# Performance work log

Hardware: AMD Instinct MI355X
Metric: run time of the kernel (lower is better)

The kernel has to match this reference:

```python
import jax, jax.numpy as jnp
import numpy as np

B, S, D = 2, 2048, 2048
H, HKV, DH = 16, 4, 128   # query heads, kv heads, head dim
N_REP = H // HKV
ROPE_BASE = 10000.0


def rotate_half(x):
    x1, x2 = x[..., : DH // 2], x[..., DH // 2 :]
    return jnp.concatenate((-x2, x1), axis=-1)


def rope_tables(seq_len, dtype=jnp.float32):
    inv_freq = 1.0 / (ROPE_BASE ** (jnp.arange(0, DH, 2, dtype=jnp.float32) / DH))
    t = jnp.arange(seq_len, dtype=jnp.float32)
    freqs = jnp.outer(t, inv_freq)                 # [S, DH/2]
    emb = jnp.concatenate((freqs, freqs), axis=-1)  # [S, DH]
    return jnp.cos(emb).astype(dtype), jnp.sin(emb).astype(dtype)


def setup_inputs() -> dict:
    key = jax.random.key(0)
    k1, k2, k3, k4, k5 = jax.random.split(key, 5)
    scale = 1.0 / np.sqrt(D)
    return {
        "hidden_states": jax.random.normal(k1, (B, S, D), dtype=jnp.float32),
        "position_ids": jnp.tile(jnp.arange(S, dtype=jnp.int32)[None, :], (B, 1)),
        "wq": jax.random.normal(k2, (D, H * DH), dtype=jnp.float32) * scale,
        "wk": jax.random.normal(k3, (D, HKV * DH), dtype=jnp.float32) * scale,
        "wv": jax.random.normal(k4, (D, HKV * DH), dtype=jnp.float32) * scale,
        "wo": jax.random.normal(k5, (H * DH, D), dtype=jnp.float32) * scale,
    }


def reference(hidden_states, position_ids, wq, wk, wv, wo):
    x = hidden_states
    b, s, _ = x.shape

    # QKV projections -> [B, H(kv), S, DH]
    q = (x @ wq).reshape(b, s, H, DH).transpose(0, 2, 1, 3)
    k = (x @ wk).reshape(b, s, HKV, DH).transpose(0, 2, 1, 3)
    v = (x @ wv).reshape(b, s, HKV, DH).transpose(0, 2, 1, 3)

    # Rotary position embedding
    cos_t, sin_t = rope_tables(s, x.dtype)
    cos = cos_t[position_ids][:, None, :, :]  # [B,1,S,DH]
    sin = sin_t[position_ids][:, None, :, :]
    q = q * cos + rotate_half(q) * sin
    k = k * cos + rotate_half(k) * sin

    # GQA: repeat KV heads to match query heads
    k = jnp.repeat(k, N_REP, axis=1)  # [B,H,S,DH]
    v = jnp.repeat(v, N_REP, axis=1)

    # Causal SDPA
    scores = jnp.einsum("bhqd,bhkd->bhqk", q, k) / jnp.sqrt(
        jnp.asarray(DH, x.dtype)
    )
    causal = jnp.tril(jnp.ones((s, s), dtype=bool))
    scores = jnp.where(causal[None, None], scores, jnp.asarray(-1e9, x.dtype))
    attn = jax.nn.softmax(scores, axis=-1)
    out = jnp.einsum("bhqk,bhkd->bhqd", attn, v)  # [B,H,S,DH]

    out = out.transpose(0, 2, 1, 3).reshape(b, s, H * DH)
    return out @ wo
```

## Files before the change

kernel.cpp:

```cpp
#include <hip/hip_runtime.h>
#include <cmath>

typedef unsigned short u16;
typedef float floatx4 __attribute__((ext_vector_type(4)));
typedef short short8 __attribute__((ext_vector_type(8)));
typedef short short4v __attribute__((ext_vector_type(4)));
typedef __bf16 bf16x8 __attribute__((ext_vector_type(8)));

#define GLOBAL_AS __attribute__((address_space(1)))
#define LDS_AS __attribute__((address_space(3)))

#define S_LEN 2048
#define D_MODEL 2048
#define NH 16
#define NKV 4
#define DHEAD 128
#define SM_SCALE 0.08838834764831843f
#define K2 (SM_SCALE * 1.4426950408889634f)

__device__ __forceinline__ u16 f2bf(float f) {
    unsigned int u = __builtin_bit_cast(unsigned int, f);
    u += 0x7fffu + ((u >> 16) & 1u);
    return (u16)(u >> 16);
}
__device__ __forceinline__ u16 f2bfr(float f) {
    unsigned int u = __builtin_bit_cast(unsigned int, f);
    return (u16)((u + 0x8000u) >> 16);
}
__device__ __forceinline__ float bf2f(u16 x) {
    unsigned int u = ((unsigned int)x) << 16;
    return __builtin_bit_cast(float, u);
}
__device__ __forceinline__ floatx4 zf4() {
    floatx4 z; z[0] = 0.f; z[1] = 0.f; z[2] = 0.f; z[3] = 0.f; return z;
}
__device__ __forceinline__ floatx4 mfma16(short8 a, short8 b, floatx4 c) {
    return __builtin_amdgcn_mfma_f32_16x16x32_bf16(
        __builtin_bit_cast(bf16x8, a), __builtin_bit_cast(bf16x8, b), c, 0, 0, 0);
}
__device__ __forceinline__ floatx4 mfma16k16(short4v a, short4v b, floatx4 c) {
    return __builtin_amdgcn_mfma_f32_16x16x16bf16_1k(a, b, c, 0, 0, 0);
}
__device__ __forceinline__ void async16(const u16* g, u16* l) {
    __builtin_amdgcn_global_load_lds((GLOBAL_AS void*)g, (LDS_AS void*)l, 16, 0, 0);
}

__global__ void cast_x_kernel(const float4* __restrict__ in, ushort4* __restrict__ out) {
    int i = blockIdx.x * 256 + threadIdx.x;
    float4 v = in[i];
    ushort4 o;
    o.x = f2bf(v.x); o.y = f2bf(v.y); o.z = f2bf(v.z); o.w = f2bf(v.w);
    out[i] = o;
}

__global__ void transpose_cast_kernel(const float* __restrict__ in, u16* __restrict__ out,
                                      int R, int C) {
    __shared__ float tile[32][33];
    int tx = threadIdx.x & 31, ty = threadIdx.x >> 5;
    int bx = blockIdx.x * 32;
    int by = blockIdx.y * 32;
#pragma unroll
    for (int i = 0; i < 32; i += 8)
        tile[ty + i][tx] = in[(size_t)(by + ty + i) * C + bx + tx];
    __syncthreads();
#pragma unroll
    for (int i = 0; i < 32; i += 8)
        out[(size_t)(bx + ty + i) * R + by + tx] = f2bf(tile[tx][ty + i]);
}

__global__ void rope_tables_kernel(float* __restrict__ cs_tab, float* __restrict__ sn_tab) {
    int idx = blockIdx.x * 256 + threadIdx.x;
    int p = idx >> 6, j = idx & 63;
    double e = (double)(2 * j) / 128.0;
    double invf = pow(10000.0, -e);
    float arg = (float)p * (float)invf;
    cs_tab[idx] = (float)cos((double)arg);
    sn_tab[idx] = (float)sin((double)arg);
}

__global__ void rope_apply_kernel(u16* __restrict__ Qb, u16* __restrict__ Kb,
                                  const int* __restrict__ pos,
                                  const float4* __restrict__ cs_tab,
                                  const float4* __restrict__ sn_tab) {
    int idx = blockIdx.x * 256 + threadIdx.x;
    int j4 = idx & 15;
    int s = (idx >> 4) & 2047;
    int r = idx >> 15;
    int hh = r % 20, b = r / 20;
    int p = pos[b * S_LEN + s];
    float4 cs = cs_tab[p * 16 + j4];
    float4 sn = sn_tab[p * 16 + j4];
    u16* base;
    if (hh < 16) base = Qb + (((size_t)(b * NH + hh)) * S_LEN + s) * DHEAD;
    else         base = Kb + (((size_t)(b * NKV + (hh - 16))) * S_LEN + s) * DHEAD;
    base += j4 * 4;
    ushort4 a = *(const ushort4*)(base);
    ushort4 c = *(const ushort4*)(base + 64);
    ushort4 oa, oc;
    float x1, x2;
    x1 = bf2f(a.x); x2 = bf2f(c.x); oa.x = f2bf(x1 * cs.x - x2 * sn.x); oc.x = f2bf(x2 * cs.x + x1 * sn.x);
    x1 = bf2f(a.y); x2 = bf2f(c.y); oa.y = f2bf(x1 * cs.y - x2 * sn.y); oc.y = f2bf(x2 * cs.y + x1 * sn.y);
    x1 = bf2f(a.z); x2 = bf2f(c.z); oa.z = f2bf(x1 * cs.z - x2 * sn.z); oc.z = f2bf(x2 * cs.z + x1 * sn.z);
    x1 = bf2f(a.w); x2 = bf2f(c.w); oa.w = f2bf(x1 * cs.w - x2 * sn.w); oc.w = f2bf(x2 * cs.w + x1 * sn.w);
    *(ushort4*)(base) = oa;
    *(ushort4*)(base + 64) = oc;
}

__device__ __forceinline__ void gemm_mainloop(const u16* __restrict__ A,
                                              const u16* __restrict__ Bt,
                                              int K, u16* ldsA, u16* ldsB,
                                              floatx4 acc[4][4]) {
    const int t = threadIdx.x;
    const int lane = t & 63, wave = t >> 6;
    const int wr = wave >> 1, wc = wave & 1;
    const int lr = lane & 15, q = lane >> 4;
    const int m0 = blockIdx.y * 128, n0 = blockIdx.x * 128;
    const int swz = q ^ ((lr >> 1) & 3);

#pragma unroll
    for (int r = 0; r < 4; ++r)
#pragma unroll
        for (int c = 0; c < 4; ++c) acc[r][c] = zf4();

    for (int k0 = 0; k0 < K; k0 += 32) {
#pragma unroll
        for (int i = 0; i < 2; ++i) {
            int ci = i * 256 + t;
            int row = ci >> 2;
            int kc = ((ci & 3) ^ ((ci >> 3) & 3)) << 3;
            async16(A + (size_t)(m0 + row) * K + k0 + kc, ldsA + (i * 256 + wave * 64) * 8);
            async16(Bt + (size_t)(n0 + row) * K + k0 + kc, ldsB + (i * 256 + wave * 64) * 8);
        }
        __syncthreads();
        short8 af[4], bfr[4];
#pragma unroll
        for (int r = 0; r < 4; ++r)
            af[r] = *(const short8*)(ldsA + (wr * 64 + r * 16 + lr) * 32 + swz * 8);
#pragma unroll
        for (int c = 0; c < 4; ++c)
            bfr[c] = *(const short8*)(ldsB + (wc * 64 + c * 16 + lr) * 32 + swz * 8);
#pragma unroll
        for (int r = 0; r < 4; ++r)
#pragma unroll
            for (int c = 0; c < 4; ++c)
                acc[r][c] = mfma16(af[r], bfr[c], acc[r][c]);
        __syncthreads();
    }
}

__global__ void qkv_gemm_kernel(const u16* __restrict__ A, const u16* __restrict__ Bt,
                                u16* __restrict__ Qb, u16* __restrict__ Kb,
                                u16* __restrict__ Vt) {
    __shared__ u16 ldsA[128 * 32];
    __shared__ u16 ldsB[128 * 32];
    floatx4 acc[4][4];
    gemm_mainloop(A, Bt, D_MODEL, ldsA, ldsB, acc);

    const int t = threadIdx.x, lane = t & 63, wave = t >> 6;
    const int wr = wave >> 1, wc = wave & 1, lr = lane & 15, q = lane >> 4;
    const int m0 = blockIdx.y * 128 + wr * 64, n0 = blockIdx.x * 128 + wc * 64;
#pragma unroll
    for (int r = 0; r < 4; ++r)
#pragma unroll
        for (int c = 0; c < 4; ++c) {
            int gc = n0 + c * 16 + lr;
#pragma unroll
            for (int rr = 0; rr < 4; ++rr) {
                int grow = m0 + r * 16 + q * 4 + rr;
                int bb = grow >> 11, s = grow & 2047;
                u16 bv = f2bf(acc[r][c][rr]);
                int d = gc & 127;
                if (gc < 2048) {
                    int hh = gc >> 7;
                    Qb[(((size_t)(bb * NH + hh)) * S_LEN + s) * DHEAD + d] = bv;
                } else if (gc < 2560) {
                    int hh = (gc - 2048) >> 7;
                    Kb[(((size_t)(bb * NKV + hh)) * S_LEN + s) * DHEAD + d] = bv;
                } else {
                    int hh = (gc - 2560) >> 7;
                    Vt[(((size_t)(bb * NKV + hh)) * DHEAD + d) * S_LEN + s] = bv;
                }
            }
        }
}

__global__ void out_gemm_kernel(const u16* __restrict__ A, const u16* __restrict__ Bt,
                                float* __restrict__ out) {
    __shared__ u16 ldsA[128 * 32];
    __shared__ u16 ldsB[128 * 32];
    floatx4 acc[4][4];
    gemm_mainloop(A, Bt, D_MODEL, ldsA, ldsB, acc);

    const int t = threadIdx.x, lane = t & 63, wave = t >> 6;
    const int wr = wave >> 1, wc = wave & 1, lr = lane & 15, q = lane >> 4;
    const int m0 = blockIdx.y * 128 + wr * 64, n0 = blockIdx.x * 128 + wc * 64;
#pragma unroll
    for (int r = 0; r < 4; ++r)
#pragma unroll
        for (int c = 0; c < 4; ++c) {
            int gc = n0 + c * 16 + lr;
#pragma unroll
            for (int rr = 0; rr < 4; ++rr) {
                int grow = m0 + r * 16 + q * 4 + rr;
                out[(size_t)grow * D_MODEL + gc] = acc[r][c][rr];
            }
        }
}

__global__ __launch_bounds__(256, 4) void fa_kernel(const u16* __restrict__ Qb,
                                                    const u16* __restrict__ Kb,
                                                    const u16* __restrict__ Vt,
                                                    u16* __restrict__ Ob) {
    __shared__ u16 ldsK[64 * 128];
    __shared__ u16 ldsV[128 * 64];

    const int t = threadIdx.x, lane = t & 63, wave = t >> 6;
    const int lr = lane & 15, q = lane >> 4;
    const int swz = lr & 7;

    const int bid = blockIdx.x;
    const int qt = 31 - (bid >> 5);
    const int bh = bid & 31;
    const int b = bh >> 4, h = bh & 15;
    const int kvh = h >> 2;

    const u16* Kp = Kb + (size_t)(b * NKV + kvh) * S_LEN * DHEAD;
    const u16* Vp = Vt + (size_t)(b * NKV + kvh) * DHEAD * S_LEN;
    const u16* Qp = Qb + ((size_t)((b * NH + h) * S_LEN) + qt * 64 + wave * 16) * DHEAD;

    short8 qf[4];
#pragma unroll
    for (int kk = 0; kk < 4; ++kk)
        qf[kk] = *(const short8*)(Qp + (size_t)lr * DHEAD + kk * 32 + q * 8);

    floatx4 accO[8];
#pragma unroll
    for (int d = 0; d < 8; ++d) accO[d] = zf4();
    float m_i = -3e38f, l_i = 0.f;

    const int nkt = qt + 1;
    for (int kt = 0; kt < nkt; ++kt) {
#pragma unroll
        for (int i = 0; i < 4; ++i) {
            int ci = i * 256 + t;
            int krow = ci >> 4, kc = ((ci & 15) ^ ((ci >> 4) & 7)) << 3;
            async16(Kp + (size_t)(kt * 64 + krow) * DHEAD + kc,
                    ldsK + (i * 256 + wave * 64) * 8);
            int dh = ci >> 3, vc = ((ci & 7) ^ ((ci >> 3) & 7)) << 3;
            async16(Vp + (size_t)dh * S_LEN + kt * 64 + vc,
                    ldsV + (i * 256 + wave * 64) * 8);
        }
        __syncthreads();

        floatx4 sc[4];
#pragma unroll
        for (int c = 0; c < 4; ++c) {
            sc[c] = zf4();
#pragma unroll
            for (int kk = 0; kk < 4; ++kk) {
                short8 kfr = *(const short8*)(ldsK + (c * 16 + lr) * DHEAD +
                                              (((kk * 4 + q) ^ swz) << 3));
                sc[c] = mfma16(kfr, qf[kk], sc[c]);
            }
        }

        if (kt == qt) {
            const int qrow = wave * 16 + lr;
#pragma unroll
            for (int c = 0; c < 4; ++c)
#pragma unroll
                for (int rr = 0; rr < 4; ++rr)
                    if (c * 16 + q * 4 + rr > qrow) sc[c][rr] = -3e38f;
        }

        float mx = -3e38f;
#pragma unroll
        for (int c = 0; c < 4; ++c)
#pragma unroll
            for (int rr = 0; rr < 4; ++rr) mx = fmaxf(mx, sc[c][rr]);
        mx = fmaxf(mx, __shfl_xor(mx, 16));
        mx = fmaxf(mx, __shfl_xor(mx, 32));
        float mnew = fmaxf(m_i, mx);
        float mk = mnew * K2;
        float alpha = __builtin_amdgcn_exp2f(fmaf(m_i, K2, -mk));
        m_i = mnew;
        float rs = 0.f;
#pragma unroll
        for (int c = 0; c < 4; ++c)
#pragma unroll
            for (int rr = 0; rr < 4; ++rr) {
                float p = __builtin_amdgcn_exp2f(fmaf(sc[c][rr], K2, -mk));
                sc[c][rr] = p;
                rs += p;
            }
        rs += __shfl_xor(rs, 16);
        rs += __shfl_xor(rs, 32);
        l_i = l_i * alpha + rs;
#pragma unroll
        for (int d = 0; d < 8; ++d) accO[d] *= alpha;

        short4v pb[4];
#pragma unroll
        for (int c = 0; c < 4; ++c) {
            pb[c][0] = (short)f2bfr(sc[c][0]);
            pb[c][1] = (short)f2bfr(sc[c][1]);
            pb[c][2] = (short)f2bfr(sc[c][2]);
            pb[c][3] = (short)f2bfr(sc[c][3]);
        }

#pragma unroll
        for (int ks = 0; ks < 4; ++ks)
#pragma unroll
            for (int d = 0; d < 8; ++d) {
                short4v vf = *(const short4v*)(ldsV + (d * 16 + lr) * 64 +
                                               (((ks * 2 + (q >> 1)) ^ swz) << 3) +
                                               (q & 1) * 4);
                accO[d] = mfma16k16(vf, pb[ks], accO[d]);
            }
        __syncthreads();
    }

    const int tok = qt * 64 + wave * 16 + lr;
    const float inv = 1.0f / l_i;
    u16* orow = Ob + ((size_t)(b * S_LEN + tok)) * (NH * DHEAD) + h * DHEAD + q * 4;
#pragma unroll
    for (int d = 0; d < 8; ++d) {
        ushort4 o;
        o.x = f2bf(accO[d][0] * inv);
        o.y = f2bf(accO[d][1] * inv);
        o.z = f2bf(accO[d][2] * inv);
        o.w = f2bf(accO[d][3] * inv);
        *(ushort4*)(orow + d * 16) = o;
    }
}

extern "C" void kernel_launch(void* const* d_in, const int* in_sizes, int n_in,
                              void* d_out, int out_size, void* d_ws, size_t ws_size,
                              hipStream_t stream) {
    const float* X  = (const float*)d_in[0];
    const int* pos  = (const int*)d_in[1];
    const float* wq = (const float*)d_in[2];
    const float* wk = (const float*)d_in[3];
    const float* wv = (const float*)d_in[4];
    const float* wo = (const float*)d_in[5];
    float* out = (float*)d_out;

    char* w = (char*)d_ws;
    u16* Xbf    = (u16*)(w);
    u16* Wqkv   = (u16*)(w + 16777216);
    u16* Wo     = (u16*)(w + 29360128);
    u16* Qb     = (u16*)(w + 37748736);
    u16* Kb     = (u16*)(w + 54525952);
    u16* Vt     = (u16*)(w + 58720256);
    u16* Ob     = (u16*)(w + 62914560);
    float* cst  = (float*)(w + 79691776);
    float* snt  = (float*)(w + 80216064);

    cast_x_kernel<<<8192, 256, 0, stream>>>((const float4*)X, (ushort4*)Xbf);
    transpose_cast_kernel<<<dim3(64, 64), 256, 0, stream>>>(wq, Wqkv, 2048, 2048);
    transpose_cast_kernel<<<dim3(16, 64), 256, 0, stream>>>(wk, Wqkv + (size_t)2048 * 2048, 2048, 512);
    transpose_cast_kernel<<<dim3(16, 64), 256, 0, stream>>>(wv, Wqkv + (size_t)2560 * 2048, 2048, 512);
    transpose_cast_kernel<<<dim3(64, 64), 256, 0, stream>>>(wo, Wo, 2048, 2048);
    rope_tables_kernel<<<512, 256, 0, stream>>>(cst, snt);
    qkv_gemm_kernel<<<dim3(24, 32), 256, 0, stream>>>(Xbf, Wqkv, Qb, Kb, Vt);
    rope_apply_kernel<<<5120, 256, 0, stream>>>(Qb, Kb, pos, (const float4*)cst, (const float4*)snt);
    fa_kernel<<<1024, 256, 0, stream>>>(Qb, Kb, Vt, Ob);
    out_gemm_kernel<<<dim3(16, 32), 256, 0, stream>>>(Ob, Wo, out);
}
```

Baseline: 326.3 us.

## Deepen GEMM K-tile, reorder attention blocks, skip redundant rescale, swizzle V layout

The shared GEMM mainloop now stages 64-wide K tiles, using a new 8-way XOR swizzle and two MFMA sub-steps per barrier pair, which halves the number of barriers and LDS refill rounds. The flash-attention grid is remapped so that each group of blocks pairs short and long causal query tiles, which should balance work across CUs. The online-softmax rescale of the accumulator is skipped when no row max increased in the wave. V is written with an XOR of the sequence index so that the half-16-byte reads in attention hit fewer LDS bank conflicts. Together these raise LDS usage and add some index arithmetic.

```diff
diff --git a/kernel.cpp b/kernel.cpp
--- a/kernel.cpp
+++ b/kernel.cpp
@@ -115,35 +115,40 @@
     const int wr = wave >> 1, wc = wave & 1;
     const int lr = lane & 15, q = lane >> 4;
     const int m0 = blockIdx.y * 128, n0 = blockIdx.x * 128;
-    const int swz = q ^ ((lr >> 1) & 3);
+    const int swz = lr & 7;
 
 #pragma unroll
     for (int r = 0; r < 4; ++r)
 #pragma unroll
         for (int c = 0; c < 4; ++c) acc[r][c] = zf4();
 
-    for (int k0 = 0; k0 < K; k0 += 32) {
-#pragma unroll
-        for (int i = 0; i < 2; ++i) {
+    for (int k0 = 0; k0 < K; k0 += 64) {
+#pragma unroll
+        for (int i = 0; i < 4; ++i) {
             int ci = i * 256 + t;
-            int row = ci >> 2;
-            int kc = ((ci & 3) ^ ((ci >> 3) & 3)) << 3;
+            int row = ci >> 3;
+            int kc = ((ci & 7) ^ (row & 7)) << 3;
             async16(A + (size_t)(m0 + row) * K + k0 + kc, ldsA + (i * 256 + wave * 64) * 8);
             async16(Bt + (size_t)(n0 + row) * K + k0 + kc, ldsB + (i * 256 + wave * 64) * 8);
         }
         __syncthreads();
-        short8 af[4], bfr[4];
-#pragma unroll
-        for (int r = 0; r < 4; ++r)
-            af[r] = *(const short8*)(ldsA + (wr * 64 + r * 16 + lr) * 32 + swz * 8);
-#pragma unroll
-        for (int c = 0; c < 4; ++c)
-            bfr[c] = *(const short8*)(ldsB + (wc * 64 + c * 16 + lr) * 32 + swz * 8);
-#pragma unroll
-        for (int r = 0; r < 4; ++r)
+#pragma unroll
+        for (int ks = 0; ks < 2; ++ks) {
+            short8 af[4], bfr[4];
+#pragma unroll
+            for (int r = 0; r < 4; ++r)
+                af[r] = *(const short8*)(ldsA + (wr * 64 + r * 16 + lr) * 64 +
+                                         (((ks * 4 + q) ^ swz) << 3));
 #pragma unroll
             for (int c = 0; c < 4; ++c)
-                acc[r][c] = mfma16(af[r], bfr[c], acc[r][c]);
+                bfr[c] = *(const short8*)(ldsB + (wc * 64 + c * 16 + lr) * 64 +
+                                          (((ks * 4 + q) ^ swz) << 3));
+#pragma unroll
+            for (int r = 0; r < 4; ++r)
+#pragma unroll
+                for (int c = 0; c < 4; ++c)
+                    acc[r][c] = mfma16(af[r], bfr[c], acc[r][c]);
+        }
         __syncthreads();
     }
 }
@@ -151,8 +156,8 @@
 __global__ void qkv_gemm_kernel(const u16* __restrict__ A, const u16* __restrict__ Bt,
                                 u16* __restrict__ Qb, u16* __restrict__ Kb,
                                 u16* __restrict__ Vt) {
-    __shared__ u16 ldsA[128 * 32];
-    __shared__ u16 ldsB[128 * 32];
+    __shared__ u16 ldsA[128 * 64];
+    __shared__ u16 ldsB[128 * 64];
     floatx4 acc[4][4];
     gemm_mainloop(A, Bt, D_MODEL, ldsA, ldsB, acc);
 
@@ -178,7 +183,8 @@
                     Kb[(((size_t)(bb * NKV + hh)) * S_LEN + s) * DHEAD + d] = bv;
                 } else {
                     int hh = (gc - 2560) >> 7;
-                    Vt[(((size_t)(bb * NKV + hh)) * DHEAD + d) * S_LEN + s] = bv;
+                    int s2 = s ^ ((d & 8) >> 1);
+                    Vt[(((size_t)(bb * NKV + hh)) * DHEAD + d) * S_LEN + s2] = bv;
                 }
             }
         }
@@ -186,8 +192,8 @@
 
 __global__ void out_gemm_kernel(const u16* __restrict__ A, const u16* __restrict__ Bt,
                                 float* __restrict__ out) {
-    __shared__ u16 ldsA[128 * 32];
-    __shared__ u16 ldsB[128 * 32];
+    __shared__ u16 ldsA[128 * 64];
+    __shared__ u16 ldsB[128 * 64];
     floatx4 acc[4][4];
     gemm_mainloop(A, Bt, D_MODEL, ldsA, ldsB, acc);
 
@@ -219,8 +225,14 @@
     const int swz = lr & 7;
 
     const int bid = blockIdx.x;
-    const int qt = 31 - (bid >> 5);
-    const int bh = bid & 31;
+    const int r4 = bid >> 8, j = bid & 255;
+    const int p = j >> 3, lo = j & 7;
+    const int bh = r4 * 8 + lo;
+    int qt;
+    if (r4 == 0) qt = p;
+    else if (r4 == 1) qt = 31 - p;
+    else if (r4 == 2) qt = p ^ 16;
+    else qt = 31 - (p ^ 16);
     const int b = bh >> 4, h = bh & 15;
     const int kvh = h >> 2;
 
@@ -282,22 +294,27 @@
         mx = fmaxf(mx, __shfl_xor(mx, 32));
         float mnew = fmaxf(m_i, mx);
         float mk = mnew * K2;
-        float alpha = __builtin_amdgcn_exp2f(fmaf(m_i, K2, -mk));
-        m_i = mnew;
+        bool anyup = __any(mnew > m_i);
         float rs = 0.f;
 #pragma unroll
         for (int c = 0; c < 4; ++c)
 #pragma unroll
             for (int rr = 0; rr < 4; ++rr) {
-                float p = __builtin_amdgcn_exp2f(fmaf(sc[c][rr], K2, -mk));
-                sc[c][rr] = p;
-                rs += p;
+                float pe = __builtin_amdgcn_exp2f(fmaf(sc[c][rr], K2, -mk));
+                sc[c][rr] = pe;
+                rs += pe;
             }
         rs += __shfl_xor(rs, 16);
         rs += __shfl_xor(rs, 32);
-        l_i = l_i * alpha + rs;
-#pragma unroll
-        for (int d = 0; d < 8; ++d) accO[d] *= alpha;
+        if (anyup) {
+            float alpha = __builtin_amdgcn_exp2f(fmaf(m_i, K2, -mk));
+            l_i = l_i * alpha + rs;
+#pragma unroll
+            for (int d = 0; d < 8; ++d) accO[d] *= alpha;
+        } else {
+            l_i += rs;
+        }
+        m_i = mnew;
 
         short4v pb[4];
 #pragma unroll
@@ -314,7 +331,7 @@
             for (int d = 0; d < 8; ++d) {
                 short4v vf = *(const short4v*)(ldsV + (d * 16 + lr) * 64 +
                                                (((ks * 2 + (q >> 1)) ^ swz) << 3) +
-                                               (q & 1) * 4);
+                                               (((q ^ (lr >> 3)) & 1) << 2));
                 accO[d] = mfma16k16(vf, pb[ks], accO[d]);
             }
         __syncthreads();
```

New measurement: 312.7 us. -4.2%, faster.
